# Kernel optimization log

Measured on AMD Instinct MI355X. Metric: run time of the kernel, lower is better.

## Reference

```python
import jax, jax.numpy as jnp
import numpy as np

N, L, H, E = 4, 4096, 8, 64
CHUNK = 128  # chunk size for the blocked causal scan
EPS = 1e-6


def elu_feature_map(x):
    # phi(x) = elu(x) + 1 (default feature map of fast-transformers)
    return jax.nn.elu(x) + 1.0


def causal_dot_product(Q, K, V, chunk=CHUNK):
    """out[n,l,h,:] = sum_{s<=l} (Q[n,l,h,:].K[n,s,h,:]) * V[n,s,h,:].
    Chunked scan over the [E,M] KV state: O(N L H E M) without an [L,L] matrix."""
    n, l, h, e = Q.shape
    m = V.shape[-1]
    nc = l // chunk

    def to_chunks(x):
        # [n, l, h, d] -> [nc, n, h, chunk, d]
        return x.reshape(n, nc, chunk, h, x.shape[-1]).transpose(1, 0, 3, 2, 4)

    q, k, v = to_chunks(Q), to_chunks(K), to_chunks(V)
    tril = jnp.tril(jnp.ones((chunk, chunk), dtype=Q.dtype))

    def step(S, xs):  # S: [n, h, e, m] running sum of k v^T
        qc, kc, vc = xs  # [n, h, chunk, e/m]
        inter = jnp.einsum('nhce,nhem->nhcm', qc, S)
        attn = jnp.einsum('nhce,nhde->nhcd', qc, kc) * tril  # intra-chunk causal
        intra = jnp.einsum('nhcd,nhdm->nhcm', attn, vc)
        S = S + jnp.einsum('nhce,nhcm->nhem', kc, vc)
        return S, inter + intra

    S0 = jnp.zeros((n, h, e, m), dtype=Q.dtype)
    _, out = jax.lax.scan(step, S0, (q, k, v))  # [nc, n, h, chunk, m]
    return out.transpose(1, 0, 3, 2, 4).reshape(n, l, h, m)


def setup_inputs() -> dict:
    key = jax.random.key(0)
    k1, k2, k3 = jax.random.split(key, 3)
    return {
        'queries': jax.random.normal(k1, (N, L, H, E), jnp.float32),
        'keys': jax.random.normal(k2, (N, L, H, E), jnp.float32),
        'values': jax.random.normal(k3, (N, L, H, E), jnp.float32),
        'key_lengths': jnp.ones((N, L), jnp.float32),  # float length mask
    }


def reference(queries, keys, values, key_lengths):
    Q = elu_feature_map(queries)
    K = elu_feature_map(keys) * key_lengths[:, :, None, None]
    # denominator: Z[n,l,h] = 1 / (Q[n,l,h] . cumsum_s<=l K[n,s,h] + eps)
    Z = 1.0 / (jnp.einsum('nlhe,nlhe->nlh', Q, jnp.cumsum(K, axis=1)) + EPS)
    V_new = causal_dot_product(Q, K, values)
    return V_new * Z[:, :, :, None]
```

## Files before the change

kernel.cpp:

```cpp
#include <hip/hip_runtime.h>
#include <math.h>

#define NN 4
#define LL 4096
#define HH 8
#define EE 64
#define CHK 64
#define GSUP 4
#define NSUP 16
#define NH (NN*HH)
#define NBLK (NH*NSUP)
#define NCH64 (LL/CHK)
#define EPSF 1e-6f

typedef float f32x4 __attribute__((ext_vector_type(4)));
typedef __bf16 bf16x8 __attribute__((ext_vector_type(8)));
typedef __bf16 bf16x4 __attribute__((ext_vector_type(4)));

__device__ __forceinline__ float phi_map(float x) {
  return x > 0.0f ? x + 1.0f : __expf(x);
}

#define MFMA(a, b, c) __builtin_amdgcn_mfma_f32_16x16x32_bf16((a), (b), (c), 0, 0, 0)

__device__ __forceinline__ int swz64(int row, int d) {
  return row * 64 + (d & 7) + 8 * ((d >> 3) ^ ((row >> 2) & 7));
}
__device__ __forceinline__ int frag64(int row, int blk) {
  return row * 64 + 8 * (blk ^ ((row >> 2) & 7));
}

#define K1_ISSUE(J, BUF) { \
  const int l0i = (sc * GSUP + (J)) * CHK; \
  _Pragma("unroll") for (int it = 0; it < 4; ++it) { \
    int f = t + 256 * it; int d = f >> 4; int c4 = (f & 15) << 2; \
    size_t gb = (((size_t)n * LL + (size_t)(l0i + d)) * HH + h) * EE + c4; \
    pk[BUF][it] = *(const float4*)(Kg + gb); \
    pv[BUF][it] = *(const float4*)(Vg + gb); \
    pl[BUF][it] = KLg[n * LL + l0i + d]; } }

#define K1_STAGE(BUF) { \
  _Pragma("unroll") for (int it = 0; it < 4; ++it) { \
    int f = t + 256 * it; int d = f >> 4; int c4 = (f & 15) << 2; \
    float klr = pl[BUF][it]; float4 kk = pk[BUF][it]; float4 vv = pv[BUF][it]; \
    float ka[4] = {phi_map(kk.x) * klr, phi_map(kk.y) * klr, phi_map(kk.z) * klr, phi_map(kk.w) * klr}; \
    float va[4] = {vv.x, vv.y, vv.z, vv.w}; \
    _Pragma("unroll") for (int jj = 0; jj < 4; ++jj) { \
      sKt[BUF][swz64(c4 + jj, d)] = (__bf16)ka[jj]; \
      sVt[BUF][swz64(c4 + jj, d)] = (__bf16)va[jj]; } } }

__global__ __launch_bounds__(256, 2) void k_chunksums(
    const float* __restrict__ Kg, const float* __restrict__ Vg,
    const float* __restrict__ KLg, __bf16* __restrict__ ScG, __bf16* __restrict__ KscG)
{
  __shared__ __bf16 sKt[2][4096];
  __shared__ __bf16 sVt[2][4096];
  const int g = blockIdx.x;
  const int sc = g & (NSUP - 1);
  const int nh = g >> 4;
  const int h = nh % HH;
  const int n = nh / HH;
  const int t = threadIdx.x;
  const int w = t >> 6;
  const int lane = t & 63;
  const int lg = lane >> 4;
  const int li = lane & 15;
  const int arow = 16 * w + li;

  float4 pk[2][4], pv[2][4];
  float pl[2][4];

  K1_ISSUE(0, 0);
  K1_STAGE(0);

  f32x4 acc[4];
  #pragma unroll
  for (int nt = 0; nt < 4; ++nt) acc[nt] = (f32x4){0.f, 0.f, 0.f, 0.f};

  bf16x8 ones;
  #pragma unroll
  for (int i = 0; i < 8; ++i) ones[i] = (__bf16)1.0f;

  #pragma unroll
  for (int j = 0; j < GSUP; ++j) {
    if (j + 1 < GSUP) K1_ISSUE(j + 1, (j + 1) & 1);
    __syncthreads();

    bf16x8 bV0 = *(const bf16x8*)&sVt[j & 1][frag64(arow, lg)];
    bf16x8 bV1 = *(const bf16x8*)&sVt[j & 1][frag64(arow, 4 + lg)];

    f32x4 accK[4];
    #pragma unroll
    for (int nt = 0; nt < 4; ++nt) accK[nt] = (f32x4){0.f, 0.f, 0.f, 0.f};

    #pragma unroll
    for (int nt = 0; nt < 4; ++nt) {
      bf16x8 a0 = *(const bf16x8*)&sKt[j & 1][frag64(li + 16 * nt, lg)];
      bf16x8 a1 = *(const bf16x8*)&sKt[j & 1][frag64(li + 16 * nt, 4 + lg)];
      acc[nt] = MFMA(a0, bV0, acc[nt]);
      acc[nt] = MFMA(a1, bV1, acc[nt]);
      if (w == 0) {
        accK[nt] = MFMA(ones, a0, accK[nt]);
        accK[nt] = MFMA(ones, a1, accK[nt]);
      }
    }
    if (w == 0 && lg == 0) {
      #pragma unroll
      for (int nt = 0; nt < 4; ++nt)
        KscG[(size_t)(g * GSUP + j) * 64 + li + 16 * nt] = (__bf16)accK[nt][0];
    }
    if (j + 1 < GSUP) K1_STAGE((j + 1) & 1);
  }

  __bf16* sp = ScG + (size_t)g * 4096;
  #pragma unroll
  for (int nt = 0; nt < 4; ++nt) {
    bf16x4 sv;
    #pragma unroll
    for (int reg = 0; reg < 4; ++reg) sv[reg] = (__bf16)acc[nt][reg];
    *(bf16x4*)(sp + arow * 64 + 16 * nt + 4 * lg) = sv;
  }
}

__global__ __launch_bounds__(256) void k_prefix(
    __bf16* __restrict__ Sc, __bf16* __restrict__ Ksc)
{
  const int bid = blockIdx.x;
  const int t = threadIdx.x;
  if (bid < NH * 16) {
    const int nh = bid >> 4;
    const int strip = bid & 15;
    const int entry = strip * 256 + t;
    __bf16 v[NSUP];
    #pragma unroll
    for (int c = 0; c < NSUP; ++c)
      v[c] = Sc[((size_t)(nh * NSUP + c) << 12) + entry];
    float run = 0.0f;
    #pragma unroll
    for (int c = 0; c < NSUP; ++c) {
      Sc[((size_t)(nh * NSUP + c) << 12) + entry] = (__bf16)run;
      run += (float)v[c];
    }
  } else {
    const int idx = (bid - NH * 16) * 256 + t;
    const int nh = idx >> 6;
    const int e = idx & 63;
    __bf16 v[NCH64];
    #pragma unroll
    for (int c = 0; c < NCH64; ++c)
      v[c] = Ksc[((size_t)(nh * NCH64 + c) << 6) + e];
    float run = 0.0f;
    #pragma unroll
    for (int c = 0; c < NCH64; ++c) {
      Ksc[((size_t)(nh * NCH64 + c) << 6) + e] = (__bf16)run;
      run += (float)v[c];
    }
  }
}

#define P2_ISSUE(CC) { \
  const int l0i = (sc * GSUP + (CC)) * CHK; \
  _Pragma("unroll") for (int it = 0; it < 4; ++it) { \
    int f = t + 256 * it; int d = f >> 4; int c4 = (f & 15) << 2; \
    size_t gb = (((size_t)n * LL + (size_t)(l0i + d)) * HH + h) * EE + c4; \
    pk[it] = *(const float4*)(Kg + gb); \
    pv[it] = *(const float4*)(Vg + gb); \
    pl[it] = KLg[n * LL + l0i + d]; } \
  { const float* qr = Qg + (((size_t)n * LL + (size_t)(l0i + arow)) * HH + h) * EE; \
    pq[0] = *(const float4*)(qr + 8 * lg); \
    pq[1] = *(const float4*)(qr + 8 * lg + 4); \
    pq[2] = *(const float4*)(qr + 32 + 8 * lg); \
    pq[3] = *(const float4*)(qr + 32 + 8 * lg + 4); } }

#define P2_STAGE(QB) { \
  _Pragma("unroll") for (int it = 0; it < 4; ++it) { \
    int f = t + 256 * it; int d = f >> 4; int c4 = (f & 15) << 2; \
    float klr = pl[it]; float4 kk = pk[it]; float4 vv = pv[it]; \
    float ka[4] = {phi_map(kk.x) * klr, phi_map(kk.y) * klr, phi_map(kk.z) * klr, phi_map(kk.w) * klr}; \
    float va[4] = {vv.x, vv.y, vv.z, vv.w}; \
    bf16x4 kv4; \
    kv4[0] = (__bf16)ka[0]; kv4[1] = (__bf16)ka[1]; kv4[2] = (__bf16)ka[2]; kv4[3] = (__bf16)ka[3]; \
    *(bf16x4*)&sKe[QB][d * 64 + 8 * ((c4 >> 3) ^ ((d >> 2) & 7)) + (c4 & 7)] = kv4; \
    _Pragma("unroll") for (int jj = 0; jj < 4; ++jj) { \
      sKt[QB][swz64(c4 + jj, d)] = (__bf16)ka[jj]; \
      sVt[QB][swz64(c4 + jj, d)] = (__bf16)va[jj]; } } \
  { float4 q0 = pq[0], q1 = pq[1], q2 = pq[2], q3 = pq[3]; \
    bf16x8 a0, a1; \
    a0[0] = (__bf16)phi_map(q0.x); a0[1] = (__bf16)phi_map(q0.y); \
    a0[2] = (__bf16)phi_map(q0.z); a0[3] = (__bf16)phi_map(q0.w); \
    a0[4] = (__bf16)phi_map(q1.x); a0[5] = (__bf16)phi_map(q1.y); \
    a0[6] = (__bf16)phi_map(q1.z); a0[7] = (__bf16)phi_map(q1.w); \
    a1[0] = (__bf16)phi_map(q2.x); a1[1] = (__bf16)phi_map(q2.y); \
    a1[2] = (__bf16)phi_map(q2.z); a1[3] = (__bf16)phi_map(q2.w); \
    a1[4] = (__bf16)phi_map(q3.x); a1[5] = (__bf16)phi_map(q3.y); \
    a1[6] = (__bf16)phi_map(q3.z); a1[7] = (__bf16)phi_map(q3.w); \
    aQ[QB][0] = a0; aQ[QB][1] = a1; } }

__global__ __launch_bounds__(256, 2) void k_pass2(
    const float* __restrict__ Qg, const float* __restrict__ Kg,
    const float* __restrict__ Vg, const float* __restrict__ KLg,
    const __bf16* __restrict__ Sp, const __bf16* __restrict__ Ksp,
    float* __restrict__ Og)
{
  __shared__ __bf16 sKe[2][4096];
  __shared__ __bf16 sKt[2][4096];
  __shared__ __bf16 sVt[2][4096];
  __shared__ __bf16 sU[2][4096];
  __shared__ __bf16 sP[4][1024];

  const int g = blockIdx.x;
  const int sc = g & (NSUP - 1);
  const int nh = g >> 4;
  const int h = nh % HH;
  const int n = nh / HH;
  const int t = threadIdx.x;
  const int w = t >> 6;
  const int lane = t & 63;
  const int lg = lane >> 4;
  const int li = lane & 15;
  const int arow = 16 * w + li;

  float4 pk[4], pv[4], pq[4];
  float pl[4];
  bf16x8 aQ[2][2];

  {
    const bf16x8* sp8 = (const bf16x8*)(Sp + (size_t)g * 4096);
    bf16x8 s0 = sp8[2 * t];
    bf16x8 s1 = sp8[2 * t + 1];
    int m = t >> 2, eb = (t & 3) * 2;
    *(bf16x8*)&sU[0][frag64(m, eb)] = s0;
    *(bf16x8*)&sU[0][frag64(m, eb + 1)] = s1;
  }

  f32x4 accS[4];
  #pragma unroll
  for (int nt = 0; nt < 4; ++nt) {
    bf16x4 sv = *(const bf16x4*)(Sp + (size_t)g * 4096 + arow * 64 + 16 * nt + 4 * lg);
    #pragma unroll
    for (int reg = 0; reg < 4; ++reg) accS[nt][reg] = (float)sv[reg];
  }

  P2_ISSUE(0);
  P2_STAGE(0);

  #pragma unroll
  for (int cc = 0; cc < GSUP; ++cc) {
    const int cb = cc & 1, nb = cb ^ 1;
    __syncthreads();

    if (cc + 1 < GSUP) P2_ISSUE(cc + 1);

    if (cc + 1 < GSUP) {
      bf16x8 bV0 = *(const bf16x8*)&sVt[cb][frag64(arow, lg)];
      bf16x8 bV1 = *(const bf16x8*)&sVt[cb][frag64(arow, 4 + lg)];
      #pragma unroll
      for (int nt = 0; nt < 4; ++nt) {
        bf16x8 aKt0 = *(const bf16x8*)&sKt[cb][frag64(li + 16 * nt, lg)];
        bf16x8 aKt1 = *(const bf16x8*)&sKt[cb][frag64(li + 16 * nt, 4 + lg)];
        accS[nt] = MFMA(aKt0, bV0, accS[nt]);
        accS[nt] = MFMA(aKt1, bV1, accS[nt]);
        bf16x4 sw;
        #pragma unroll
        for (int reg = 0; reg < 4; ++reg) sw[reg] = (__bf16)accS[nt][reg];
        *(bf16x4*)&sU[nb][arow * 64 + 8 * ((2 * nt + (lg >> 1)) ^ ((arow >> 2) & 7)) + 4 * (lg & 1)] = sw;
      }
    }

    bf16x8 aQ0 = aQ[cb][0], aQ1 = aQ[cb][1];

    f32x4 acc[4];
    #pragma unroll
    for (int nt = 0; nt < 4; ++nt) {
      acc[nt] = (f32x4){0.f, 0.f, 0.f, 0.f};
      bf16x8 aS0 = *(const bf16x8*)&sU[cb][frag64(li + 16 * nt, lg)];
      bf16x8 aS1 = *(const bf16x8*)&sU[cb][frag64(li + 16 * nt, 4 + lg)];
      acc[nt] = MFMA(aS0, aQ0, acc[nt]);
      acc[nt] = MFMA(aS1, aQ1, acc[nt]);
    }

    const __bf16* kb = Ksp + (size_t)(g * GSUP + cc) * 64;
    bf16x8 ks0 = *(const bf16x8*)(kb + 8 * lg);
    bf16x8 ks1 = *(const bf16x8*)(kb + 32 + 8 * lg);
    float dv = 0.0f;
    #pragma unroll
    for (int i = 0; i < 8; ++i) {
      dv += (float)aQ0[i] * (float)ks0[i];
      dv += (float)aQ1[i] * (float)ks1[i];
    }
    dv += __shfl_xor(dv, 16);
    dv += __shfl_xor(dv, 32);

    f32x4 at2[4];
    #pragma unroll
    for (int nt = 0; nt < 4; ++nt) at2[nt] = (f32x4){0.f, 0.f, 0.f, 0.f};
    for (int nt = 0; nt <= w; ++nt) {
      bf16x8 aK0 = *(const bf16x8*)&sKe[cb][frag64(li + 16 * nt, lg)];
      bf16x8 aK1 = *(const bf16x8*)&sKe[cb][frag64(li + 16 * nt, 4 + lg)];
      at2[nt] = MFMA(aK0, aQ0, at2[nt]);
      at2[nt] = MFMA(aK1, aQ1, at2[nt]);
    }

    float rs = 0.0f;
    #pragma unroll
    for (int nt = 0; nt < 4; ++nt) {
      bf16x4 pw;
      #pragma unroll
      for (int reg = 0; reg < 4; ++reg) {
        int kk = 16 * nt + 4 * lg + reg;
        float av = (kk <= arow) ? at2[nt][reg] : 0.0f;
        rs += av;
        pw[reg] = (__bf16)av;
      }
      *(bf16x4*)&sP[w][li * 64 + 8 * ((2 * nt + (lg >> 1)) ^ (li & 7)) + 4 * (lg & 1)] = pw;
    }
    rs += __shfl_xor(rs, 16);
    rs += __shfl_xor(rs, 32);

    if (cc + 1 < GSUP) P2_STAGE(nb);

    {
      bf16x8 bP0 = *(const bf16x8*)&sP[w][li * 64 + 8 * (lg ^ (li & 7))];
      bf16x8 bP1 = *(const bf16x8*)&sP[w][li * 64 + 8 * ((4 + lg) ^ (li & 7))];
      #pragma unroll
      for (int nt = 0; nt < 4; ++nt) {
        bf16x8 aV0 = *(const bf16x8*)&sVt[cb][frag64(li + 16 * nt, lg)];
        bf16x8 aV1 = *(const bf16x8*)&sVt[cb][frag64(li + 16 * nt, 4 + lg)];
        acc[nt] = MFMA(aV0, bP0, acc[nt]);
        acc[nt] = MFMA(aV1, bP1, acc[nt]);
      }
    }

    const int l0 = (sc * GSUP + cc) * CHK;
    {
      float inv = 1.0f / (dv + rs + EPSF);
      size_t ob = (((size_t)n * LL + (size_t)(l0 + arow)) * HH + h) * EE;
      #pragma unroll
      for (int nt = 0; nt < 4; ++nt) {
        float4 o = make_float4(acc[nt][0] * inv, acc[nt][1] * inv,
                               acc[nt][2] * inv, acc[nt][3] * inv);
        *(float4*)(Og + ob + 16 * nt + 4 * lg) = o;
      }
    }
  }
}

extern "C" void kernel_launch(void* const* d_in, const int* in_sizes, int n_in,
                              void* d_out, int out_size, void* d_ws, size_t ws_size,
                              hipStream_t stream) {
  const float* Qg  = (const float*)d_in[0];
  const float* Kg  = (const float*)d_in[1];
  const float* Vg  = (const float*)d_in[2];
  const float* KLg = (const float*)d_in[3];
  float* Og = (float*)d_out;

  __bf16* Sc  = (__bf16*)d_ws;
  __bf16* Ksc = (__bf16*)((char*)d_ws + (size_t)NBLK * 4096 * 2);

  hipLaunchKernelGGL(k_chunksums, dim3(NBLK), dim3(256), 0, stream, Kg, Vg, KLg, Sc, Ksc);
  hipLaunchKernelGGL(k_prefix, dim3(NH * 16 + 8), dim3(256), 0, stream, Sc, Ksc);
  hipLaunchKernelGGL(k_pass2, dim3(NBLK), dim3(256), 0, stream, Qg, Kg, Vg, KLg, Sc, Ksc, Og);
}
```

Baseline: 47.29 us.

## Fuse prefix scan into pass2 by summing preceding chunk states per block

Removes the separate k_prefix launch. Each pass2 block now builds its own exclusive prefix by summing the chunk-sum state matrices of all earlier superchunks for its (n,h), plus a running K-sum kept in shared memory as fp32. This drops one kernel launch and its global read/write round trip. In exchange, later blocks do redundant loads, up to 15×8KB each, so work becomes imbalanced across blocks. The first Q/K/V load is issued earlier to overlap with that summation.

```diff
diff --git a/kernel.cpp b/kernel.cpp
--- a/kernel.cpp
+++ b/kernel.cpp
@@ -10,7 +10,6 @@
 #define NSUP 16
 #define NH (NN*HH)
 #define NBLK (NH*NSUP)
-#define NCH64 (LL/CHK)
 #define EPSF 1e-6f
 
 typedef float f32x4 __attribute__((ext_vector_type(4)));
@@ -119,42 +118,6 @@
     #pragma unroll
     for (int reg = 0; reg < 4; ++reg) sv[reg] = (__bf16)acc[nt][reg];
     *(bf16x4*)(sp + arow * 64 + 16 * nt + 4 * lg) = sv;
-  }
-}
-
-__global__ __launch_bounds__(256) void k_prefix(
-    __bf16* __restrict__ Sc, __bf16* __restrict__ Ksc)
-{
-  const int bid = blockIdx.x;
-  const int t = threadIdx.x;
-  if (bid < NH * 16) {
-    const int nh = bid >> 4;
-    const int strip = bid & 15;
-    const int entry = strip * 256 + t;
-    __bf16 v[NSUP];
-    #pragma unroll
-    for (int c = 0; c < NSUP; ++c)
-      v[c] = Sc[((size_t)(nh * NSUP + c) << 12) + entry];
-    float run = 0.0f;
-    #pragma unroll
-    for (int c = 0; c < NSUP; ++c) {
-      Sc[((size_t)(nh * NSUP + c) << 12) + entry] = (__bf16)run;
-      run += (float)v[c];
-    }
-  } else {
-    const int idx = (bid - NH * 16) * 256 + t;
-    const int nh = idx >> 6;
-    const int e = idx & 63;
-    __bf16 v[NCH64];
-    #pragma unroll
-    for (int c = 0; c < NCH64; ++c)
-      v[c] = Ksc[((size_t)(nh * NCH64 + c) << 6) + e];
-    float run = 0.0f;
-    #pragma unroll
-    for (int c = 0; c < NCH64; ++c) {
-      Ksc[((size_t)(nh * NCH64 + c) << 6) + e] = (__bf16)run;
-      run += (float)v[c];
-    }
   }
 }
 
@@ -199,7 +162,7 @@
 __global__ __launch_bounds__(256, 2) void k_pass2(
     const float* __restrict__ Qg, const float* __restrict__ Kg,
     const float* __restrict__ Vg, const float* __restrict__ KLg,
-    const __bf16* __restrict__ Sp, const __bf16* __restrict__ Ksp,
+    const __bf16* __restrict__ Sc, const __bf16* __restrict__ Ksc,
     float* __restrict__ Og)
 {
   __shared__ __bf16 sKe[2][4096];
@@ -207,10 +170,12 @@
   __shared__ __bf16 sVt[2][4096];
   __shared__ __bf16 sU[2][4096];
   __shared__ __bf16 sP[4][1024];
+  __shared__ float sKl[GSUP][64];
 
   const int g = blockIdx.x;
   const int sc = g & (NSUP - 1);
   const int nh = g >> 4;
+  const int g0 = nh * NSUP;
   const int h = nh % HH;
   const int n = nh / HH;
   const int t = threadIdx.x;
@@ -224,30 +189,60 @@
   float pl[4];
   bf16x8 aQ[2][2];
 
+  P2_ISSUE(0);
+
   {
-    const bf16x8* sp8 = (const bf16x8*)(Sp + (size_t)g * 4096);
-    bf16x8 s0 = sp8[2 * t];
-    bf16x8 s1 = sp8[2 * t + 1];
+    float fb[16];
+    #pragma unroll
+    for (int i = 0; i < 16; ++i) fb[i] = 0.0f;
+    for (int p = 0; p < sc; ++p) {
+      const bf16x8* sp8 = (const bf16x8*)(Sc + (size_t)(g0 + p) * 4096);
+      bf16x8 s0 = sp8[2 * t];
+      bf16x8 s1 = sp8[2 * t + 1];
+      #pragma unroll
+      for (int i = 0; i < 8; ++i) {
+        fb[i] += (float)s0[i];
+        fb[8 + i] += (float)s1[i];
+      }
+    }
+    bf16x8 b0, b1;
+    #pragma unroll
+    for (int i = 0; i < 8; ++i) {
+      b0[i] = (__bf16)fb[i];
+      b1[i] = (__bf16)fb[8 + i];
+    }
     int m = t >> 2, eb = (t & 3) * 2;
-    *(bf16x8*)&sU[0][frag64(m, eb)] = s0;
-    *(bf16x8*)&sU[0][frag64(m, eb + 1)] = s1;
-  }
+    *(bf16x8*)&sU[0][frag64(m, eb)] = b0;
+    *(bf16x8*)&sU[0][frag64(m, eb + 1)] = b1;
+  }
+
+  if (t < 64) {
+    float run = 0.0f;
+    for (int p = 0; p < sc * GSUP; ++p)
+      run += (float)Ksc[(size_t)(g0 * GSUP + p) * 64 + t];
+    #pragma unroll
+    for (int j = 0; j < GSUP; ++j) {
+      sKl[j][t] = run;
+      run += (float)Ksc[(size_t)(g * GSUP + j) * 64 + t];
+    }
+  }
+
+  P2_STAGE(0);
 
   f32x4 accS[4];
-  #pragma unroll
-  for (int nt = 0; nt < 4; ++nt) {
-    bf16x4 sv = *(const bf16x4*)(Sp + (size_t)g * 4096 + arow * 64 + 16 * nt + 4 * lg);
-    #pragma unroll
-    for (int reg = 0; reg < 4; ++reg) accS[nt][reg] = (float)sv[reg];
-  }
-
-  P2_ISSUE(0);
-  P2_STAGE(0);
 
   #pragma unroll
   for (int cc = 0; cc < GSUP; ++cc) {
     const int cb = cc & 1, nb = cb ^ 1;
     __syncthreads();
+
+    if (cc == 0) {
+      #pragma unroll
+      for (int nt = 0; nt < 4; ++nt)
+        #pragma unroll
+        for (int reg = 0; reg < 4; ++reg)
+          accS[nt][reg] = (float)sU[0][swz64(arow, 16 * nt + 4 * lg + reg)];
+    }
 
     if (cc + 1 < GSUP) P2_ISSUE(cc + 1);
 
@@ -279,14 +274,11 @@
       acc[nt] = MFMA(aS1, aQ1, acc[nt]);
     }
 
-    const __bf16* kb = Ksp + (size_t)(g * GSUP + cc) * 64;
-    bf16x8 ks0 = *(const bf16x8*)(kb + 8 * lg);
-    bf16x8 ks1 = *(const bf16x8*)(kb + 32 + 8 * lg);
     float dv = 0.0f;
     #pragma unroll
     for (int i = 0; i < 8; ++i) {
-      dv += (float)aQ0[i] * (float)ks0[i];
-      dv += (float)aQ1[i] * (float)ks1[i];
+      dv += (float)aQ0[i] * sKl[cc][8 * lg + i];
+      dv += (float)aQ1[i] * sKl[cc][32 + 8 * lg + i];
     }
     dv += __shfl_xor(dv, 16);
     dv += __shfl_xor(dv, 32);
@@ -358,6 +350,5 @@
   __bf16* Ksc = (__bf16*)((char*)d_ws + (size_t)NBLK * 4096 * 2);
 
   hipLaunchKernelGGL(k_chunksums, dim3(NBLK), dim3(256), 0, stream, Kg, Vg, KLg, Sc, Ksc);
-  hipLaunchKernelGGL(k_prefix, dim3(NH * 16 + 8), dim3(256), 0, stream, Sc, Ksc);
   hipLaunchKernelGGL(k_pass2, dim3(NBLK), dim3(256), 0, stream, Qg, Kg, Vg, KLg, Sc, Ksc, Og);
 }
```

Result: slower. 58.70 us (+24.1%).
